# Performance work log

Measured on AMD Instinct MI355X. Metric: run time of the kernel, lower is better.

## Reference

```python
import jax, jax.numpy as jnp
import numpy as np

NUM_PHRASE = 8
HDIM = 256
NUM_HEADS = 8
NUM_LAYERS = 3
MIN_DIST = 2


def sine_pos(mask, num_feats, temperature=10000.0):
    # PositionEmbeddingSine (1D, DETR-style, normalize=False)
    B, L = mask.shape
    x_embed = jnp.cumsum(mask.astype(jnp.float32), axis=1)            # [B,L]
    dim_t = jnp.arange(num_feats, dtype=jnp.float32)
    dim_t = temperature ** (2.0 * jnp.floor(dim_t / 2.0) / num_feats)
    pos = x_embed[:, :, None] / dim_t                                  # [B,L,C]
    pos = jnp.stack([jnp.sin(pos[:, :, 0::2]), jnp.cos(pos[:, :, 1::2])], axis=3)
    return pos.reshape(B, L, num_feats)


def layer_norm(x, g, b, eps=1e-5):
    mu = jnp.mean(x, axis=-1, keepdims=True)
    var = jnp.mean((x - mu) ** 2, axis=-1, keepdims=True)
    return (x - mu) / jnp.sqrt(var + eps) * g + b


def mha(q, k, v, key_mask, in_w, in_b, out_w, out_b, nheads):
    # torch nn.MultiheadAttention (batch_first, eval/no-dropout), averaged attn weights
    B, Lq, C = q.shape
    Dh = C // nheads
    qp = (q @ in_w[:, :C] + in_b[:C]).reshape(B, Lq, nheads, Dh)
    kp = (k @ in_w[:, C:2 * C] + in_b[C:2 * C]).reshape(B, -1, nheads, Dh)
    vp = (v @ in_w[:, 2 * C:] + in_b[2 * C:]).reshape(B, -1, nheads, Dh)
    scores = jnp.einsum('bqhd,bkhd->bhqk', qp, kp) / jnp.sqrt(jnp.float32(Dh))
    scores = jnp.where(key_mask[:, None, None, :], scores, -jnp.inf)
    attn = jax.nn.softmax(scores, axis=-1)
    out = jnp.einsum('bhqk,bkhd->bqhd', attn, vp).reshape(B, Lq, C)
    return out @ out_w + out_b, jnp.mean(attn, axis=1)


def cross_attention(x, y, mask, qw, qb, kvw, kvb, inw, inb, ow, ob, g0, b0, lw, lb, g1, b1):
    C = x.shape[-1]
    q = x @ qw + qb
    kv = y @ kvw + kvb
    k, v = kv[..., :C], kv[..., C:]
    q_att, attn = mha(q, k, v, mask, inw, inb, ow, ob, NUM_HEADS)
    x = layer_norm(x + q_att, g0, b0)
    update = jax.nn.relu(x @ lw + lb)
    x = layer_norm(x + update, g1, b1)
    return x, attn


def _select_one(entropy_b, mask_b):
    # greedy highest-entropy selection with min-distance suppression (1D NMS)
    P, MD = NUM_PHRASE, MIN_DIST
    score = jnp.where(mask_b, entropy_b, -jnp.inf)
    order = jnp.argsort(-score).astype(jnp.int32)   # valid indices first, descending entropy

    def step(carry, idx):
        sel, cnt = carry
        dists = jnp.where(sel >= 0, jnp.abs(idx - sel), 1000000)
        ok = mask_b[idx] & (cnt < P) & (jnp.min(dists) >= MD)
        new_sel = jnp.where(ok, sel.at[jnp.minimum(cnt, P - 1)].set(idx), sel)
        return (new_sel, cnt + ok.astype(jnp.int32)), None

    init = (jnp.full((P,), -1, jnp.int32), jnp.int32(0))
    (sel, cnt), _ = jax.lax.scan(step, init, order)
    last = sel[jnp.maximum(cnt - 1, 0)]
    return jnp.where(jnp.arange(P) < cnt, sel, last)   # pad by repeating last


def phrase_generate(txt_emb, txt_mask, video_feats, video_mask,
                    word_proj_w, word_proj_b, video_proj_w, video_proj_b,
                    q_w, q_b, kv_w, kv_b, in_w, in_b, out_w, out_b,
                    ln0_g, ln0_b, lin_w, lin_b, ln1_g, ln1_b, eos_slot):
    B, L, C = txt_emb.shape
    word_emb = txt_emb[:, 1:]
    word_mask = txt_mask[:, 1:]
    word_pe = word_emb + sine_pos(word_mask, C)

    # word importance via video cross-attention entropy
    wp = word_pe @ word_proj_w + word_proj_b                      # [B,Lw,C]
    vp = video_feats @ video_proj_w + video_proj_b                # [B,T,C]
    sim = jnp.einsum('blc,btc->blt', wp, vp)                      # [B,Lw,T]
    sim = jnp.where(video_mask[:, None, :], sim, -jnp.inf)
    attn_weights = jax.nn.softmax(sim, axis=2)
    entropy = -jnp.sum(attn_weights * jnp.log(attn_weights + 1e-6), axis=2)  # [B,Lw]

    sel = jax.vmap(_select_one)(entropy, word_mask)               # [B,P] int32
    phrase_slot = jnp.take_along_axis(word_pe, sel[:, :, None], axis=1)      # [B,P,C]

    slot_sim = None
    for i in range(NUM_LAYERS):
        phrase_slot, slot_sim = cross_attention(
            phrase_slot, word_pe, word_mask,
            q_w[i], q_b[i], kv_w[i], kv_b[i], in_w[i], in_b[i], out_w[i], out_b[i],
            ln0_g[i], ln0_b[i], lin_w[i], lin_b[i], ln1_g[i], ln1_b[i])

    eos = jnp.broadcast_to(eos_slot, (B, 1, C))
    return phrase_slot, attn_weights, slot_sim, eos


def setup_inputs() -> dict:
    key = jax.random.key(0)
    ks = jax.random.split(key, 16)
    B, L, T, C, NL = 128, 257, 1024, HDIM, NUM_LAYERS
    s = 0.02
    inp = {
        'txt_emb': jax.random.normal(ks[0], (B, L, C), jnp.float32),
        'txt_mask': jnp.ones((B, L), jnp.bool_),
        'video_feats': jax.random.normal(ks[1], (B, T, C), jnp.float32),
        'video_mask': jnp.ones((B, T), jnp.bool_),
        'word_proj_w': jax.random.normal(ks[2], (C, C)) * s,
        'word_proj_b': jnp.zeros((C,)),
        'video_proj_w': jax.random.normal(ks[3], (C, C)) * s,
        'video_proj_b': jnp.zeros((C,)),
        'q_w': jax.random.normal(ks[4], (NL, C, C)) * s,
        'q_b': jnp.zeros((NL, C)),
        'kv_w': jax.random.normal(ks[5], (NL, C, 2 * C)) * s,
        'kv_b': jnp.zeros((NL, 2 * C)),
        'in_w': jax.random.normal(ks[6], (NL, C, 3 * C)) * s,
        'in_b': jnp.zeros((NL, 3 * C)),
        'out_w': jax.random.normal(ks[7], (NL, C, C)) * s,
        'out_b': jnp.zeros((NL, C)),
        'ln0_g': jnp.ones((NL, C)),
        'ln0_b': jnp.zeros((NL, C)),
        'lin_w': jax.random.normal(ks[8], (NL, C, C)) * s,
        'lin_b': jnp.zeros((NL, C)),
        'ln1_g': jnp.ones((NL, C)),
        'ln1_b': jnp.zeros((NL, C)),
        'eos_slot': jax.random.normal(ks[9], (1, 1, C)),
    }
    return inp


def reference(txt_emb, txt_mask, video_feats, video_mask,
              word_proj_w, word_proj_b, video_proj_w, video_proj_b,
              q_w, q_b, kv_w, kv_b, in_w, in_b, out_w, out_b,
              ln0_g, ln0_b, lin_w, lin_b, ln1_g, ln1_b, eos_slot):
    return phrase_generate(txt_emb, txt_mask, video_feats, video_mask,
                           word_proj_w, word_proj_b, video_proj_w, video_proj_b,
                           q_w, q_b, kv_w, kv_b, in_w, in_b, out_w, out_b,
                           ln0_g, ln0_b, lin_w, lin_b, ln1_g, ln1_b, eos_slot)
```

## Files before the change

kernel.cpp:

```cpp
#include <hip/hip_runtime.h>
#include <math.h>

#define BB 128
#define LFULL 257
#define LW 256
#define TT 1024
#define CC 256
#define NH 8
#define DHD 32
#define PP 8
#define NLAY 3

typedef __bf16 bf16x8 __attribute__((ext_vector_type(8)));
typedef __bf16 bf16x4 __attribute__((ext_vector_type(4)));
typedef float  f32x4  __attribute__((ext_vector_type(4)));

__device__ __forceinline__ float blockReduceSum(float v, volatile float* lds) {
#pragma unroll
    for (int m = 32; m >= 1; m >>= 1) v += __shfl_xor(v, m);
    __syncthreads();
    if ((threadIdx.x & 63) == 0) lds[threadIdx.x >> 6] = v;
    __syncthreads();
    return lds[0] + lds[1] + lds[2] + lds[3];
}
__device__ __forceinline__ float blockReduceMax(float v, volatile float* lds) {
#pragma unroll
    for (int m = 32; m >= 1; m >>= 1) v = fmaxf(v, __shfl_xor(v, m));
    __syncthreads();
    if ((threadIdx.x & 63) == 0) lds[threadIdx.x >> 6] = v;
    __syncthreads();
    return fmaxf(fmaxf(lds[0], lds[1]), fmaxf(lds[2], lds[3]));
}


__device__ __forceinline__ int ldsoff(int row, int col) {
    return ((row >> 6) << 11)
         + ((((row >> 4) & 3) << 2) + (col >> 3)) * 128
         + ((row & 15) << 3) + (col & 7);
}

template<int SPLIT, int B_F32, int OUT_SPLIT>
__global__ __launch_bounds__(512, 4) void gemm_mfma(
    const __bf16* __restrict__ Ahi, const __bf16* __restrict__ Alo, int lda, long long sA,
    const void* __restrict__ Bhp, const void* __restrict__ Blp, int ldb, long long sB,
    const float* __restrict__ bias,
    float* __restrict__ Cf, __bf16* __restrict__ Chi, __bf16* __restrict__ Clo,
    int ldc, long long sC, int M, int N, int K)
{
    __shared__ __bf16 sAh[2][4096];
    __shared__ __bf16 sAl[SPLIT ? 2 : 1][SPLIT ? 4096 : 1];
    __shared__ __bf16 sBh[2][4096];
    __shared__ __bf16 sBl[SPLIT ? 2 : 1][SPLIT ? 4096 : 1];

    const int tid = threadIdx.x;
    const int n0 = blockIdx.x * 128;
    const int m0 = blockIdx.y * 128;
    const long long bz = blockIdx.z;
    const __bf16* Ah = Ahi + bz * sA;
    const __bf16* Al = SPLIT ? (Alo + bz * sA) : nullptr;

    const int wv = tid >> 6, lane = tid & 63;
    const int wm = (wv & 1) << 6;
    const int wn = (wv >> 1) << 5;
    const int lr = lane & 15, quad = lane >> 4;

    const int sr = tid >> 2;
    const int sc = (tid & 3) << 3;
    const int soff = ldsoff(sr, sc);
    const long long aoff = (long long)(m0 + sr) * lda + sc;
    const long long boff = (long long)(n0 + sr) * ldb + sc;

    const int abase = ((wm >> 6) << 11) + (lane << 3);
    const int bbase = ((wn >> 6) << 11) + (((wn >> 4) & 3) << 9) + (lane << 3);

    bf16x8 rAh0, rAl0, rBh0, rBl0; float4 rBa0, rBb0;
    bf16x8 rAh1, rAl1, rBh1, rBl1; float4 rBa1, rBb1;

#define LOADR(S, k0) do {                                                         \
    rAh##S = *(const bf16x8*)&Ah[aoff + (k0)];                                    \
    if constexpr (SPLIT) rAl##S = *(const bf16x8*)&Al[aoff + (k0)];               \
    if constexpr (B_F32) {                                                        \
        const float* Bf_ = (const float*)Bhp + bz * sB;                           \
        rBa##S = *(const float4*)&Bf_[boff + (k0)];                               \
        rBb##S = *(const float4*)&Bf_[boff + (k0) + 4];                           \
    } else {                                                                      \
        const __bf16* Bh_ = (const __bf16*)Bhp + bz * sB;                         \
        rBh##S = *(const bf16x8*)&Bh_[boff + (k0)];                               \
        if constexpr (SPLIT) {                                                    \
            const __bf16* Bl_ = (const __bf16*)Blp + bz * sB;                     \
            rBl##S = *(const bf16x8*)&Bl_[boff + (k0)];                           \
        }                                                                         \
    } } while (0)

#define WRITEL(S, buf) do {                                                       \
    *(bf16x8*)&sAh[buf][soff] = rAh##S;                                           \
    if constexpr (SPLIT) *(bf16x8*)&sAl[buf][soff] = rAl##S;                      \
    if constexpr (B_F32) {                                                        \
        bf16x8 h8_, l8_;                                                          \
        h8_[0] = (__bf16)rBa##S.x; l8_[0] = (__bf16)(rBa##S.x - (float)h8_[0]);   \
        h8_[1] = (__bf16)rBa##S.y; l8_[1] = (__bf16)(rBa##S.y - (float)h8_[1]);   \
        h8_[2] = (__bf16)rBa##S.z; l8_[2] = (__bf16)(rBa##S.z - (float)h8_[2]);   \
        h8_[3] = (__bf16)rBa##S.w; l8_[3] = (__bf16)(rBa##S.w - (float)h8_[3]);   \
        h8_[4] = (__bf16)rBb##S.x; l8_[4] = (__bf16)(rBb##S.x - (float)h8_[4]);   \
        h8_[5] = (__bf16)rBb##S.y; l8_[5] = (__bf16)(rBb##S.y - (float)h8_[5]);   \
        h8_[6] = (__bf16)rBb##S.z; l8_[6] = (__bf16)(rBb##S.z - (float)h8_[6]);   \
        h8_[7] = (__bf16)rBb##S.w; l8_[7] = (__bf16)(rBb##S.w - (float)h8_[7]);   \
        *(bf16x8*)&sBh[buf][soff] = h8_;                                          \
        *(bf16x8*)&sBl[buf][soff] = l8_;                                          \
    } else {                                                                      \
        *(bf16x8*)&sBh[buf][soff] = rBh##S;                                       \
        if constexpr (SPLIT) *(bf16x8*)&sBl[buf][soff] = rBl##S;                  \
    } } while (0)

    f32x4 acc[4][2];
#pragma unroll
    for (int i = 0; i < 4; ++i)
#pragma unroll
        for (int j = 0; j < 2; ++j) acc[i][j] = (f32x4)(0.f);

    auto DOMFMA = [&](int buf) {
        bf16x8 fbh[2], fbl[2];
#pragma unroll
        for (int j = 0; j < 2; ++j) {
            fbh[j] = *(const bf16x8*)&sBh[buf][bbase + j * 512];
            if constexpr (SPLIT)
                fbl[j] = *(const bf16x8*)&sBl[buf][bbase + j * 512];
        }
#pragma unroll
        for (int i = 0; i < 4; ++i) {
            bf16x8 fah = *(const bf16x8*)&sAh[buf][abase + i * 512];
            if constexpr (SPLIT) {
                bf16x8 fal = *(const bf16x8*)&sAl[buf][abase + i * 512];
#pragma unroll
                for (int j = 0; j < 2; ++j) {
                    acc[i][j] = __builtin_amdgcn_mfma_f32_16x16x32_bf16(fal, fbh[j], acc[i][j], 0, 0, 0);
                    acc[i][j] = __builtin_amdgcn_mfma_f32_16x16x32_bf16(fah, fbl[j], acc[i][j], 0, 0, 0);
                    acc[i][j] = __builtin_amdgcn_mfma_f32_16x16x32_bf16(fah, fbh[j], acc[i][j], 0, 0, 0);
                }
            } else {
#pragma unroll
                for (int j = 0; j < 2; ++j)
                    acc[i][j] = __builtin_amdgcn_mfma_f32_16x16x32_bf16(fah, fbh[j], acc[i][j], 0, 0, 0);
            }
        }
    };

    const int nt = K >> 5;
    LOADR(0, 0);
    if (nt > 1) LOADR(1, 32);
    WRITEL(0, 0);
    if (nt > 2) LOADR(0, 64);
    __syncthreads();

    for (int t = 0; t < nt; t += 2) {
        DOMFMA(0);
        if (t + 1 < nt) {
            WRITEL(1, 1);
            if (t + 3 < nt) LOADR(1, (t + 3) << 5);
            __syncthreads();
            DOMFMA(1);
            if (t + 2 < nt) {
                WRITEL(0, 0);
                if (t + 4 < nt) LOADR(0, (t + 4) << 5);
                __syncthreads();
            }
        }
    }
#undef LOADR
#undef WRITEL

#pragma unroll
    for (int i = 0; i < 4; ++i)
#pragma unroll
        for (int j = 0; j < 2; ++j) {
            int col = n0 + wn + j * 16 + lr;
            int row0 = m0 + wm + i * 16 + quad * 4;
            float bv = bias ? bias[col] : 0.f;
#pragma unroll
            for (int r = 0; r < 4; ++r) {
                float v = acc[i][j][r] + bv;
                long long off = (long long)(row0 + r) * ldc + col + bz * sC;
                if constexpr (OUT_SPLIT) {
                    __bf16 h = (__bf16)v;
                    Chi[off] = h;
                    Clo[off] = (__bf16)(v - (float)h);
                } else {
                    Cf[off] = v;
                }
            }
        }
}

#define GTS 64
#define GKT 16
#define GPAD 68

template<int TRANSB, int RELU, int TRANSC>
__global__ __launch_bounds__(256) void gemm_f32(
    const float* __restrict__ A, int lda, long long sA,
    const float* __restrict__ Bm, int ldb, long long sB,
    const float* __restrict__ bias,
    float* __restrict__ C, int ldc, long long sC,
    int M, int N, int K)
{
    __shared__ float As[GKT][GPAD];
    __shared__ float Bs[GKT][GPAD];
    const int tid = threadIdx.x;
    const int tx = tid & 15, ty = tid >> 4;
    const int n0 = blockIdx.x * GTS;
    const int m0 = blockIdx.y * GTS;
    const long long bz = blockIdx.z;
    const float* Ab = A + bz * sA;
    const float* Bb = Bm + bz * sB;
    float* Cb = C + bz * sC;

    const int lr = tid >> 2;
    const int lc = (tid & 3) << 2;
    const int br = tid >> 4;
    const int bc = (tid & 15) << 2;

    float acc[4][4] = {};

    for (int k0 = 0; k0 < K; k0 += GKT) {
        float4 a = *(const float4*)&Ab[(long long)(m0 + lr) * lda + k0 + lc];
        As[lc + 0][lr] = a.x; As[lc + 1][lr] = a.y;
        As[lc + 2][lr] = a.z; As[lc + 3][lr] = a.w;
        if (TRANSB) {
            float4 b = *(const float4*)&Bb[(long long)(n0 + lr) * ldb + k0 + lc];
            Bs[lc + 0][lr] = b.x; Bs[lc + 1][lr] = b.y;
            Bs[lc + 2][lr] = b.z; Bs[lc + 3][lr] = b.w;
        } else {
            float4 b = *(const float4*)&Bb[(long long)(k0 + br) * ldb + n0 + bc];
            *(float4*)&Bs[br][bc] = b;
        }
        __syncthreads();
#pragma unroll
        for (int k = 0; k < GKT; ++k) {
            float4 av = *(const float4*)&As[k][ty << 2];
            float4 bv = *(const float4*)&Bs[k][tx << 2];
            float ar[4] = {av.x, av.y, av.z, av.w};
            float brr[4] = {bv.x, bv.y, bv.z, bv.w};
#pragma unroll
            for (int i = 0; i < 4; ++i)
#pragma unroll
                for (int j = 0; j < 4; ++j)
                    acc[i][j] = fmaf(ar[i], brr[j], acc[i][j]);
        }
        __syncthreads();
    }

    float bbr[4] = {0.f, 0.f, 0.f, 0.f};
    if (bias) {
        float4 bb = *(const float4*)&bias[n0 + (tx << 2)];
        bbr[0] = bb.x; bbr[1] = bb.y; bbr[2] = bb.z; bbr[3] = bb.w;
    }
#pragma unroll
    for (int i = 0; i < 4; ++i) {
#pragma unroll
        for (int j = 0; j < 4; ++j) {
            float o = acc[i][j] + bbr[j];
            if (RELU) o = fmaxf(o, 0.f);
            if (TRANSC)
                Cb[(long long)(n0 + (tx << 2) + j) * ldc + m0 + (ty << 2) + i] = o;
            else
                Cb[(long long)(m0 + (ty << 2) + i) * ldc + n0 + (tx << 2) + j] = o;
        }
    }
}


__global__ __launch_bounds__(256) void cumsum_kernel(
    const int* __restrict__ tm, int* __restrict__ cums)
{
    int b = blockIdx.x, c = threadIdx.x;
    int lane = c & 63;
    int v = (tm[(long long)b * LFULL + 1 + c] != 0) ? 1 : 0;
#pragma unroll
    for (int off = 1; off < 64; off <<= 1) {
        int t = __shfl_up(v, off);
        if (lane >= off) v += t;
    }
    __shared__ int wsum[4];
    if (lane == 63) wsum[c >> 6] = v;
    __syncthreads();
    int w = c >> 6, add = 0;
    for (int i = 0; i < w; ++i) add += wsum[i];
    cums[b * LW + c] = v + add;
}

__global__ __launch_bounds__(256) void pe_table_kernel(float* __restrict__ petab)
{
    int n = blockIdx.x;
    int c = threadIdx.x;
    int i2 = c & ~1;
    float freq = powf(10000.0f, (float)i2 / (float)CC);
    float arg = (float)n / freq;
    petab[n * CC + c] = (c & 1) ? cosf(arg) : sinf(arg);
}

__global__ __launch_bounds__(256) void word_pe2_kernel(
    const float* __restrict__ te, const int* __restrict__ cums,
    const float* __restrict__ petab,
    __bf16* __restrict__ whi, __bf16* __restrict__ wlo)
{
    int g = blockIdx.x * 256 + threadIdx.x;
    int c0 = (g & 63) << 2;
    int l  = (g >> 6) & 255;
    int b  = g >> 14;
    int cnt = cums[b * LW + l];
    float4 s = *(const float4*)&te[((long long)(b * LFULL + 1 + l)) * CC + c0];
    float4 p = *(const float4*)&petab[cnt * CC + c0];
    float v0 = s.x + p.x, v1 = s.y + p.y, v2 = s.z + p.z, v3 = s.w + p.w;
    bf16x4 h, lo;
    h[0] = (__bf16)v0; lo[0] = (__bf16)(v0 - (float)h[0]);
    h[1] = (__bf16)v1; lo[1] = (__bf16)(v1 - (float)h[1]);
    h[2] = (__bf16)v2; lo[2] = (__bf16)(v2 - (float)h[2]);
    h[3] = (__bf16)v3; lo[3] = (__bf16)(v3 - (float)h[3]);
    long long o = ((long long)(b * LW + l)) * CC + c0;
    *(bf16x4*)&whi[o] = h;
    *(bf16x4*)&wlo[o] = lo;
}

__global__ __launch_bounds__(256) void split_transpose_kernel(
    const float* __restrict__ W, __bf16* __restrict__ hi, __bf16* __restrict__ lo)
{
    int n = blockIdx.x, k = threadIdx.x;
    float v = W[(long long)k * CC + n];
    __bf16 h = (__bf16)v;
    hi[(long long)n * CC + k] = h;
    lo[(long long)n * CC + k] = (__bf16)(v - (float)h);
}
__global__ __launch_bounds__(256) void split_plain_kernel(
    const float* __restrict__ W, __bf16* __restrict__ hi, __bf16* __restrict__ lo)
{
    int g = blockIdx.x * 256 + threadIdx.x;
    float v = W[g];
    __bf16 h = (__bf16)v;
    hi[g] = h;
    lo[g] = (__bf16)(v - (float)h);
}
__global__ __launch_bounds__(256) void cvt_bf16_kernel(
    const float* __restrict__ src, __bf16* __restrict__ dst)
{
    int g = blockIdx.x * 256 + threadIdx.x;
    dst[g] = (__bf16)src[g];
}

__global__ __launch_bounds__(256) void softmax_entropy_kernel(
    float* __restrict__ attn, const int* __restrict__ vmask,
    float* __restrict__ ent)
{
    __shared__ float lds[4];
    long long row = blockIdx.x;
    int b = blockIdx.x >> 8;
    float* p = attn + row * TT;
    const int* m = vmask + (long long)b * TT;
    int t4 = threadIdx.x * 4;
    float4 v = *(const float4*)&p[t4];
    int4 mm4 = *(const int4*)&m[t4];
    float x[4];
    x[0] = mm4.x ? v.x : -INFINITY;
    x[1] = mm4.y ? v.y : -INFINITY;
    x[2] = mm4.z ? v.z : -INFINITY;
    x[3] = mm4.w ? v.w : -INFINITY;
    float mx = fmaxf(fmaxf(x[0], x[1]), fmaxf(x[2], x[3]));
    mx = blockReduceMax(mx, lds);
    float e[4];
    float ps = 0.f;
#pragma unroll
    for (int j = 0; j < 4; ++j) { e[j] = expf(x[j] - mx); ps += e[j]; }
    float sum = blockReduceSum(ps, lds);
    float q[4];
    float ce = 0.f;
#pragma unroll
    for (int j = 0; j < 4; ++j) {
        q[j] = e[j] / sum;
        ce += q[j] * logf(q[j] + 1e-6f);
    }
    ce = blockReduceSum(ce, lds);
    *(float4*)&p[t4] = make_float4(q[0], q[1], q[2], q[3]);
    if (threadIdx.x == 0) ent[row] = -ce;
}

__global__ __launch_bounds__(256) void select_kernel(
    const float* __restrict__ ent, const int* __restrict__ tm,
    int* __restrict__ sel)
{
    int b = blockIdx.x;
    int l = threadIdx.x;
    __shared__ float sc[LW];
    __shared__ int ord[LW];
    __shared__ unsigned char mk[LW];
    mk[l] = (tm[(long long)b * LFULL + 1 + l] != 0);
    sc[l] = mk[l] ? ent[(long long)b * LW + l] : -INFINITY;
    __syncthreads();
    float mys = sc[l];
    int r = 0;
    for (int j = 0; j < LW; ++j) {
        float s = sc[j];
        r += (s > mys) || (s == mys && j < l);
    }
    ord[r] = l;
    __syncthreads();
    if (l == 0) {
        int chosen[PP];
        int cnt = 0;
        for (int t = 0; t < LW; ++t) {
            int idx = ord[t];
            if (!mk[idx]) continue;
            if (cnt >= PP) break;
            bool ok = true;
            for (int s2 = 0; s2 < cnt; ++s2) {
                int d = idx - chosen[s2];
                if (d < 0) d = -d;
                if (d < 2) ok = false;
            }
            if (ok) chosen[cnt++] = idx;
        }
        int last = (cnt > 0) ? chosen[cnt - 1] : -1;
        for (int p = 0; p < PP; ++p)
            sel[b * PP + p] = (p < cnt) ? chosen[p] : last;
    }
}

__global__ __launch_bounds__(256) void gather_kernel(
    const __bf16* __restrict__ whi, const __bf16* __restrict__ wlo,
    const int* __restrict__ sel, float* __restrict__ x0)
{
    int g = blockIdx.x * 256 + threadIdx.x;
    int b = g >> 11;
    int p = (g >> 8) & 7;
    int c = g & 255;
    int idx = sel[b * PP + p];
    if (idx < 0) idx = 0;
    long long off = ((long long)b * LW + idx) * CC + c;
    x0[g] = (float)whi[off] + (float)wlo[off];
}

__global__ __launch_bounds__(256) void eff_bias_kernel(
    const float* __restrict__ q_b, const float* __restrict__ kv_b,
    const float* __restrict__ in_w, const float* __restrict__ in_b,
    float* __restrict__ BQE_all, float* __restrict__ bkv3)
{
    int i = blockIdx.x / 3;
    int role = blockIdx.x % 3;
    int n = threadIdx.x;
    const float* inw = in_w + (long long)i * 196608;
    const float* inb = in_b + (long long)i * 768;
    const float* srcb;
    int co;
    float* dst;
    if (role == 0)      { srcb = q_b + i * 256;        co = 0;   dst = BQE_all + i * 256; }
    else if (role == 1) { srcb = kv_b + i * 512;       co = 256; dst = bkv3 + i * 512; }
    else                { srcb = kv_b + i * 512 + 256; co = 512; dst = bkv3 + i * 512 + 256; }
    float s = inb[co + n];
#pragma unroll 8
    for (int k = 0; k < CC; ++k)
        s = fmaf(srcb[k], inw[(long long)k * 768 + co + n], s);
    dst[n] = s;
}

__global__ __launch_bounds__(256) void attn_scores_kernel(
    const float* __restrict__ qp, const float* __restrict__ KV,
    const int* __restrict__ tm, float* __restrict__ attn)
{
    int b = blockIdx.x, h = blockIdx.y;
    int tid = threadIdx.x;
    __shared__ float qs[PP][DHD];
    __shared__ float sc[PP][LW];
    __shared__ float mxs[PP], sms[PP];
    {
        int q = tid >> 5, d = tid & 31;
        qs[q][d] = qp[((long long)(b * PP + q)) * CC + h * DHD + d];
    }
    __syncthreads();
    const float* kr = KV + ((long long)(b * LW + tid)) * 512 + h * DHD;
    float kreg[DHD];
#pragma unroll
    for (int j = 0; j < 8; ++j) {
        float4 f = *(const float4*)&kr[j * 4];
        kreg[j * 4 + 0] = f.x; kreg[j * 4 + 1] = f.y;
        kreg[j * 4 + 2] = f.z; kreg[j * 4 + 3] = f.w;
    }
    bool mk = tm[(long long)b * LFULL + 1 + tid] != 0;
#pragma unroll
    for (int q = 0; q < PP; ++q) {
        float s = 0.f;
#pragma unroll
        for (int d = 0; d < DHD; ++d) s = fmaf(qs[q][d], kreg[d], s);
        sc[q][tid] = mk ? s * 0.17677669529663687f : -INFINITY;
    }
    __syncthreads();
    {
        int q = tid >> 5, j = tid & 31;
        float m = -INFINITY;
        for (int kk = j; kk < LW; kk += 32) m = fmaxf(m, sc[q][kk]);
#pragma unroll
        for (int mm = 16; mm >= 1; mm >>= 1) m = fmaxf(m, __shfl_xor(m, mm, 32));
        float s = 0.f;
        for (int kk = j; kk < LW; kk += 32) s += expf(sc[q][kk] - m);
#pragma unroll
        for (int mm = 16; mm >= 1; mm >>= 1) s += __shfl_xor(s, mm, 32);
        if (j == 0) { mxs[q] = m; sms[q] = s; }
    }
    __syncthreads();
#pragma unroll
    for (int q = 0; q < PP; ++q) {
        float pv = expf(sc[q][tid] - mxs[q]) / sms[q];
        attn[(((long long)(b * NH + h)) * PP + q) * LW + tid] = pv;
    }
}

__global__ __launch_bounds__(256) void attn_out_kernel(
    const float* __restrict__ attn, const float* __restrict__ KV,
    float* __restrict__ aout)
{
    int b = blockIdx.x, q = blockIdx.y;
    int c = threadIdx.x, h = c >> 5;
    __shared__ float att[NH][LW];
#pragma unroll
    for (int hh = 0; hh < NH; ++hh)
        att[hh][c] = attn[(((long long)(b * NH + hh)) * PP + q) * LW + c];
    __syncthreads();
    const float* vpb = KV + ((long long)b * LW) * 512 + 256 + c;
    float acc = 0.f;
#pragma unroll 8
    for (int k = 0; k < LW; ++k)
        acc = fmaf(att[h][k], vpb[(long long)k * 512], acc);
    aout[((long long)(b * PP + q)) * CC + c] = acc;
}

__global__ __launch_bounds__(256) void slot_sim_kernel(
    const float* __restrict__ attn, float* __restrict__ outs)
{
    int b = blockIdx.x, q = blockIdx.y, k = threadIdx.x;
    float s = 0.f;
#pragma unroll
    for (int h = 0; h < NH; ++h)
        s += attn[(((long long)(b * NH + h)) * PP + q) * LW + k];
    outs[((long long)(b * PP + q)) * LW + k] = s * 0.125f;
}

__global__ __launch_bounds__(256) void ln_residual_kernel(
    const float* __restrict__ xin, const float* __restrict__ add,
    const float* __restrict__ g, const float* __restrict__ bta,
    float* __restrict__ out)
{
    __shared__ float lds[4];
    int r = blockIdx.x, c = threadIdx.x;
    long long idx = (long long)r * CC + c;
    float v = xin[idx] + add[idx];
    float s = blockReduceSum(v, lds);
    float mu = s * (1.0f / (float)CC);
    float d = v - mu;
    float var = blockReduceSum(d * d, lds) * (1.0f / (float)CC);
    out[idx] = d / sqrtf(var + 1e-5f) * g[c] + bta[c];
}

__global__ __launch_bounds__(256) void eos_kernel(
    const float* __restrict__ eos, float* __restrict__ outp)
{
    outp[(long long)blockIdx.x * CC + threadIdx.x] = eos[threadIdx.x];
}

extern "C" void kernel_launch(void* const* d_in, const int* in_sizes, int n_in,
                              void* d_out, int out_size, void* d_ws, size_t ws_size,
                              hipStream_t stream) {
    const float* txt_emb     = (const float*)d_in[0];
    const int*   txt_mask    = (const int*)d_in[1];
    const float* video_feats = (const float*)d_in[2];
    const int*   video_mask  = (const int*)d_in[3];
    const float* word_proj_w = (const float*)d_in[4];
    const float* word_proj_b = (const float*)d_in[5];
    const float* video_proj_w = (const float*)d_in[6];
    const float* q_w   = (const float*)d_in[8];
    const float* q_b   = (const float*)d_in[9];
    const float* kv_w  = (const float*)d_in[10];
    const float* kv_b  = (const float*)d_in[11];
    const float* in_w  = (const float*)d_in[12];
    const float* in_b  = (const float*)d_in[13];
    const float* out_w = (const float*)d_in[14];
    const float* out_b = (const float*)d_in[15];
    const float* ln0_g = (const float*)d_in[16];
    const float* ln0_b = (const float*)d_in[17];
    const float* lin_w = (const float*)d_in[18];
    const float* lin_b = (const float*)d_in[19];
    const float* ln1_g = (const float*)d_in[20];
    const float* ln1_b = (const float*)d_in[21];
    const float* eos_slot = (const float*)d_in[22];

    float* ws = (float*)d_ws;
    __bf16* wpe_hi = (__bf16*)(ws + 0LL);
    __bf16* wpe_lo = (__bf16*)(ws + 4194304LL);
    __bf16* wp_hi  = (__bf16*)(ws + 8388608LL);
    __bf16* wp_lo  = (__bf16*)(ws + 12582912LL);
    __bf16* U_hi   = (__bf16*)(ws + 16777216LL);
    __bf16* U_lo   = (__bf16*)(ws + 20971520LL);
    float*  KV     = ws + 8388608LL;
    float* ent     = ws + 25165824LL;
    int*   sel     = (int*)(ws + 25198592LL);
    float* x0      = ws + 25199616LL;
    float* x1      = ws + 25461760LL;
    float* xmid    = ws + 25723904LL;
    float* qp      = ws + 25986048LL;
    float* attnw   = ws + 26248192LL;
    float* aout    = ws + 28345344LL;
    float* qatt    = ws + 28607488LL;
    float* upd     = ws + 28869632LL;
    float* WQE_all = ws + 29131776LL;
    float* BQE_all = ws + 29328384LL;
    float* WT3f    = ws + 29329152LL;
    __bf16* WT3    = (__bf16*)(ws + 29722368LL);
    float* bkv3    = ws + 29918976LL;
    __bf16* WPT_hi = (__bf16*)(ws + 29920512LL);
    __bf16* WPT_lo = (__bf16*)(ws + 29953280LL);
    __bf16* VPS_hi = (__bf16*)(ws + 29986048LL);
    __bf16* VPS_lo = (__bf16*)(ws + 30018816LL);

    int*   cums  = (int*)(ws + 8388608LL);
    float* petab = ws + 8421376LL;

    float* outp     = (float*)d_out;
    float* out_ps   = outp;
    float* out_attn = outp + 262144LL;
    float* out_slot = outp + 33816576LL;
    float* out_eos  = outp + 34078720LL;

    cumsum_kernel<<<dim3(BB), dim3(256), 0, stream>>>(txt_mask, cums);
    pe_table_kernel<<<dim3(257), dim3(256), 0, stream>>>(petab);
    word_pe2_kernel<<<dim3(8192), dim3(256), 0, stream>>>(txt_emb, cums, petab, wpe_hi, wpe_lo);
    split_transpose_kernel<<<dim3(256), dim3(256), 0, stream>>>(word_proj_w, WPT_hi, WPT_lo);
    split_plain_kernel<<<dim3(256), dim3(256), 0, stream>>>(video_proj_w, VPS_hi, VPS_lo);
    gemm_mfma<1,0,1><<<dim3(2,256,1), dim3(512), 0, stream>>>(
        wpe_hi, wpe_lo, 256, 0, WPT_hi, WPT_lo, 256, 0, word_proj_b,
        nullptr, wp_hi, wp_lo, 256, 0, 32768, 256, 256);
    gemm_mfma<1,0,1><<<dim3(2,256,1), dim3(512), 0, stream>>>(
        wp_hi, wp_lo, 256, 0, VPS_hi, VPS_lo, 256, 0, nullptr,
        nullptr, U_hi, U_lo, 256, 0, 32768, 256, 256);
    gemm_mfma<1,1,0><<<dim3(8,2,BB), dim3(512), 0, stream>>>(
        U_hi, U_lo, 256, 65536LL, video_feats, nullptr, 256, 262144LL, nullptr,
        out_attn, nullptr, nullptr, 1024, 262144LL, 256, 1024, 256);
    softmax_entropy_kernel<<<dim3(32768), dim3(256), 0, stream>>>(out_attn, video_mask, ent);
    select_kernel<<<dim3(BB), dim3(256), 0, stream>>>(ent, txt_mask, sel);
    gather_kernel<<<dim3(1024), dim3(256), 0, stream>>>(wpe_hi, wpe_lo, sel, x0);

    gemm_f32<0,0,0><<<dim3(4,4,3), dim3(256), 0, stream>>>(
        q_w,256,65536LL, in_w,768,196608LL, nullptr, WQE_all,256,65536LL, 256,256,256);
    gemm_f32<0,0,1><<<dim3(4,4,3), dim3(256), 0, stream>>>(
        kv_w,512,131072LL, in_w+256,768,196608LL, nullptr, WT3f,256,131072LL, 256,256,256);
    gemm_f32<0,0,1><<<dim3(4,4,3), dim3(256), 0, stream>>>(
        kv_w+256,512,131072LL, in_w+512,768,196608LL, nullptr, WT3f+65536,256,131072LL, 256,256,256);
    eff_bias_kernel<<<dim3(9), dim3(256), 0, stream>>>(q_b, kv_b, in_w, in_b, BQE_all, bkv3);
    cvt_bf16_kernel<<<dim3(1536), dim3(256), 0, stream>>>(WT3f, (__bf16*)WT3);

    float* X = x0;
    for (int i = 0; i < NLAY; ++i) {
        const float* ow  = out_w + (long long)i * 65536;
        const float* ob  = out_b + (long long)i * 256;
        const float* g0  = ln0_g + (long long)i * 256;
        const float* b0  = ln0_b + (long long)i * 256;
        const float* lw  = lin_w + (long long)i * 65536;
        const float* lb  = lin_b + (long long)i * 256;
        const float* g1  = ln1_g + (long long)i * 256;
        const float* b1  = ln1_b + (long long)i * 256;

        gemm_mfma<0,0,0><<<dim3(4,256,1), dim3(512), 0, stream>>>(
            wpe_hi, nullptr, 256, 0, WT3 + (long long)i * 131072, nullptr, 256, 0,
            bkv3 + i * 512, KV, nullptr, nullptr, 512, 0, 32768, 512, 256);

        gemm_f32<0,0,0><<<dim3(4,16,1), dim3(256), 0, stream>>>(
            X,256,0, WQE_all + (long long)i*65536,256,0, BQE_all + i*256, qp,256,0, 1024,256,256);

        attn_scores_kernel<<<dim3(BB,NH), dim3(256), 0, stream>>>(qp, KV, txt_mask, attnw);
        attn_out_kernel<<<dim3(BB,PP), dim3(256), 0, stream>>>(attnw, KV, aout);
        if (i == NLAY - 1)
            slot_sim_kernel<<<dim3(BB,PP), dim3(256), 0, stream>>>(attnw, out_slot);

        gemm_f32<0,0,0><<<dim3(4,16,1), dim3(256), 0, stream>>>(
            aout,256,0, ow,256,0, ob, qatt,256,0, 1024,256,256);
        ln_residual_kernel<<<dim3(1024), dim3(256), 0, stream>>>(X, qatt, g0, b0, xmid);
        gemm_f32<0,1,0><<<dim3(4,16,1), dim3(256), 0, stream>>>(
            xmid,256,0, lw,256,0, lb, upd,256,0, 1024,256,256);
        float* Xout = (i == NLAY - 1) ? out_ps : ((X == x0) ? x1 : x0);
        ln_residual_kernel<<<dim3(1024), dim3(256), 0, stream>>>(xmid, upd, g1, b1, Xout);
        X = Xout;
    }
    eos_kernel<<<dim3(BB), dim3(256), 0, stream>>>(eos_slot, out_eos);
}
```

Baseline: 889.9 us.

## Fuse similarity GEMM with masked softmax and entropy into one kernel

Replaces the batched similarity GEMM plus the separate softmax/entropy pass with a single kernel. Each 1024-thread block computes a 32x1024 score tile in registers with split-bf16 MFMAs, then does the masked softmax and entropy reductions through shuffles and LDS before writing the probabilities once. This removes a full write and read-back of the 128x256x1024 fp32 attention tensor and one kernel launch. In exchange, each block holds a full row of 1024 columns, so there is one block per 32 rows, every block re-reads its batch's video features, and the large block size may limit occupancy.

```diff
diff --git a/kernel.cpp b/kernel.cpp
--- a/kernel.cpp
+++ b/kernel.cpp
@@ -191,6 +191,204 @@
         }
 }
 
+__global__ __launch_bounds__(1024, 4) void sim_fused_kernel(
+    const __bf16* __restrict__ Uhi, const __bf16* __restrict__ Ulo,
+    const float* __restrict__ video, const int* __restrict__ vmask,
+    float* __restrict__ attn, float* __restrict__ ent)
+{
+    __shared__ __bf16 sAh[8192];
+    __shared__ __bf16 sAl[8192];
+    __shared__ float red[16][32];
+
+    const int tid = threadIdx.x;
+    const int m0 = blockIdx.x * 32;
+    const long long z = blockIdx.y;
+    const int wv = tid >> 6, lane = tid & 63;
+    const int lr = lane & 15, quad = lane >> 4;
+    const int wn = wv << 6;
+
+    const __bf16* Ah = Uhi + z * 65536;
+    const __bf16* Al = Ulo + z * 65536;
+    const float*  Bf = video + z * 262144;
+
+    {
+        int srow = (((tid >> 6) & 1) << 4) + (tid & 15);
+        int sk0  = ((tid >> 7) << 5) + (((tid >> 4) & 3) << 3);
+        long long goff = (long long)(m0 + srow) * CC + sk0;
+        *(bf16x8*)&sAh[tid * 8] = *(const bf16x8*)&Ah[goff];
+        *(bf16x8*)&sAl[tid * 8] = *(const bf16x8*)&Al[goff];
+    }
+
+    bool mk[4];
+#pragma unroll
+    for (int j = 0; j < 4; ++j)
+        mk[j] = vmask[z * TT + wn + j * 16 + lr] != 0;
+
+    f32x4 acc[2][4];
+#pragma unroll
+    for (int mf = 0; mf < 2; ++mf)
+#pragma unroll
+        for (int j = 0; j < 4; ++j) acc[mf][j] = (f32x4)(0.f);
+
+    __syncthreads();
+
+    const long long bb = (long long)(wn + lr) * CC + quad * 8;
+#pragma unroll
+    for (int ks = 0; ks < 8; ++ks) {
+        float4 b0[4], b1[4];
+#pragma unroll
+        for (int j = 0; j < 4; ++j) {
+            const float* p = Bf + bb + j * 4096 + ks * 32;
+            b0[j] = *(const float4*)p;
+            b1[j] = *(const float4*)(p + 4);
+        }
+        bf16x8 fah[2], fal[2];
+#pragma unroll
+        for (int mf = 0; mf < 2; ++mf) {
+            fah[mf] = *(const bf16x8*)&sAh[ks * 1024 + mf * 512 + lane * 8];
+            fal[mf] = *(const bf16x8*)&sAl[ks * 1024 + mf * 512 + lane * 8];
+        }
+#pragma unroll
+        for (int j = 0; j < 4; ++j) {
+            bf16x8 bh, bl;
+            bh[0] = (__bf16)b0[j].x; bl[0] = (__bf16)(b0[j].x - (float)bh[0]);
+            bh[1] = (__bf16)b0[j].y; bl[1] = (__bf16)(b0[j].y - (float)bh[1]);
+            bh[2] = (__bf16)b0[j].z; bl[2] = (__bf16)(b0[j].z - (float)bh[2]);
+            bh[3] = (__bf16)b0[j].w; bl[3] = (__bf16)(b0[j].w - (float)bh[3]);
+            bh[4] = (__bf16)b1[j].x; bl[4] = (__bf16)(b1[j].x - (float)bh[4]);
+            bh[5] = (__bf16)b1[j].y; bl[5] = (__bf16)(b1[j].y - (float)bh[5]);
+            bh[6] = (__bf16)b1[j].z; bl[6] = (__bf16)(b1[j].z - (float)bh[6]);
+            bh[7] = (__bf16)b1[j].w; bl[7] = (__bf16)(b1[j].w - (float)bh[7]);
+#pragma unroll
+            for (int mf = 0; mf < 2; ++mf) {
+                acc[mf][j] = __builtin_amdgcn_mfma_f32_16x16x32_bf16(fal[mf], bh, acc[mf][j], 0, 0, 0);
+                acc[mf][j] = __builtin_amdgcn_mfma_f32_16x16x32_bf16(fah[mf], bl, acc[mf][j], 0, 0, 0);
+                acc[mf][j] = __builtin_amdgcn_mfma_f32_16x16x32_bf16(fah[mf], bh, acc[mf][j], 0, 0, 0);
+            }
+        }
+    }
+
+    float pmax[2][4];
+#pragma unroll
+    for (int mf = 0; mf < 2; ++mf)
+#pragma unroll
+        for (int rr = 0; rr < 4; ++rr) {
+            float m = -INFINITY;
+#pragma unroll
+            for (int j = 0; j < 4; ++j)
+                if (mk[j]) m = fmaxf(m, acc[mf][j][rr]);
+            pmax[mf][rr] = m;
+        }
+#pragma unroll
+    for (int d = 1; d < 16; d <<= 1)
+#pragma unroll
+        for (int mf = 0; mf < 2; ++mf)
+#pragma unroll
+            for (int rr = 0; rr < 4; ++rr)
+                pmax[mf][rr] = fmaxf(pmax[mf][rr], __shfl_xor(pmax[mf][rr], d));
+    if (lr == 0)
+#pragma unroll
+        for (int mf = 0; mf < 2; ++mf)
+#pragma unroll
+            for (int rr = 0; rr < 4; ++rr)
+                red[wv][mf * 16 + quad * 4 + rr] = pmax[mf][rr];
+    __syncthreads();
+    float rmax[2][4];
+#pragma unroll
+    for (int mf = 0; mf < 2; ++mf)
+#pragma unroll
+        for (int rr = 0; rr < 4; ++rr) {
+            float m = -INFINITY;
+            for (int w = 0; w < 16; ++w) m = fmaxf(m, red[w][mf * 16 + quad * 4 + rr]);
+            rmax[mf][rr] = m;
+        }
+    __syncthreads();
+
+    float psum[2][4];
+#pragma unroll
+    for (int mf = 0; mf < 2; ++mf)
+#pragma unroll
+        for (int rr = 0; rr < 4; ++rr) psum[mf][rr] = 0.f;
+#pragma unroll
+    for (int mf = 0; mf < 2; ++mf)
+#pragma unroll
+        for (int j = 0; j < 4; ++j)
+#pragma unroll
+            for (int rr = 0; rr < 4; ++rr) {
+                float xv = mk[j] ? acc[mf][j][rr] : -INFINITY;
+                float ev = expf(xv - rmax[mf][rr]);
+                acc[mf][j][rr] = ev;
+                psum[mf][rr] += ev;
+            }
+#pragma unroll
+    for (int d = 1; d < 16; d <<= 1)
+#pragma unroll
+        for (int mf = 0; mf < 2; ++mf)
+#pragma unroll
+            for (int rr = 0; rr < 4; ++rr)
+                psum[mf][rr] += __shfl_xor(psum[mf][rr], d);
+    if (lr == 0)
+#pragma unroll
+        for (int mf = 0; mf < 2; ++mf)
+#pragma unroll
+            for (int rr = 0; rr < 4; ++rr)
+                red[wv][mf * 16 + quad * 4 + rr] = psum[mf][rr];
+    __syncthreads();
+    float rsum[2][4];
+#pragma unroll
+    for (int mf = 0; mf < 2; ++mf)
+#pragma unroll
+        for (int rr = 0; rr < 4; ++rr) {
+            float s = 0.f;
+            for (int w = 0; w < 16; ++w) s += red[w][mf * 16 + quad * 4 + rr];
+            rsum[mf][rr] = s;
+        }
+    __syncthreads();
+
+    float pce[2][4];
+#pragma unroll
+    for (int mf = 0; mf < 2; ++mf)
+#pragma unroll
+        for (int rr = 0; rr < 4; ++rr) pce[mf][rr] = 0.f;
+#pragma unroll
+    for (int mf = 0; mf < 2; ++mf)
+#pragma unroll
+        for (int rr = 0; rr < 4; ++rr) {
+            long long rowg = z * (long long)LW + m0 + mf * 16 + quad * 4 + rr;
+#pragma unroll
+            for (int j = 0; j < 4; ++j) {
+                float q = acc[mf][j][rr] / rsum[mf][rr];
+                attn[rowg * TT + wn + j * 16 + lr] = q;
+                pce[mf][rr] += q * logf(q + 1e-6f);
+            }
+        }
+#pragma unroll
+    for (int d = 1; d < 16; d <<= 1)
+#pragma unroll
+        for (int mf = 0; mf < 2; ++mf)
+#pragma unroll
+            for (int rr = 0; rr < 4; ++rr)
+                pce[mf][rr] += __shfl_xor(pce[mf][rr], d);
+    if (lr == 0)
+#pragma unroll
+        for (int mf = 0; mf < 2; ++mf)
+#pragma unroll
+            for (int rr = 0; rr < 4; ++rr)
+                red[wv][mf * 16 + quad * 4 + rr] = pce[mf][rr];
+    __syncthreads();
+    if (wv == 0 && lr == 0) {
+#pragma unroll
+        for (int mf = 0; mf < 2; ++mf)
+#pragma unroll
+            for (int rr = 0; rr < 4; ++rr) {
+                int row = mf * 16 + quad * 4 + rr;
+                float s = 0.f;
+                for (int w = 0; w < 16; ++w) s += red[w][row];
+                ent[z * (long long)LW + m0 + row] = -s;
+            }
+    }
+}
+
 #define GTS 64
 #define GKT 16
 #define GPAD 68
@@ -267,7 +465,6 @@
         }
     }
 }
-
 
 __global__ __launch_bounds__(256) void cumsum_kernel(
     const int* __restrict__ tm, int* __restrict__ cums)
@@ -344,42 +541,6 @@
 {
     int g = blockIdx.x * 256 + threadIdx.x;
     dst[g] = (__bf16)src[g];
-}
-
-__global__ __launch_bounds__(256) void softmax_entropy_kernel(
-    float* __restrict__ attn, const int* __restrict__ vmask,
-    float* __restrict__ ent)
-{
-    __shared__ float lds[4];
-    long long row = blockIdx.x;
-    int b = blockIdx.x >> 8;
-    float* p = attn + row * TT;
-    const int* m = vmask + (long long)b * TT;
-    int t4 = threadIdx.x * 4;
-    float4 v = *(const float4*)&p[t4];
-    int4 mm4 = *(const int4*)&m[t4];
-    float x[4];
-    x[0] = mm4.x ? v.x : -INFINITY;
-    x[1] = mm4.y ? v.y : -INFINITY;
-    x[2] = mm4.z ? v.z : -INFINITY;
-    x[3] = mm4.w ? v.w : -INFINITY;
-    float mx = fmaxf(fmaxf(x[0], x[1]), fmaxf(x[2], x[3]));
-    mx = blockReduceMax(mx, lds);
-    float e[4];
-    float ps = 0.f;
-#pragma unroll
-    for (int j = 0; j < 4; ++j) { e[j] = expf(x[j] - mx); ps += e[j]; }
-    float sum = blockReduceSum(ps, lds);
-    float q[4];
-    float ce = 0.f;
-#pragma unroll
-    for (int j = 0; j < 4; ++j) {
-        q[j] = e[j] / sum;
-        ce += q[j] * logf(q[j] + 1e-6f);
-    }
-    ce = blockReduceSum(ce, lds);
-    *(float4*)&p[t4] = make_float4(q[0], q[1], q[2], q[3]);
-    if (threadIdx.x == 0) ent[row] = -ce;
 }
 
 __global__ __launch_bounds__(256) void select_kernel(
@@ -637,10 +798,8 @@
     gemm_mfma<1,0,1><<<dim3(2,256,1), dim3(512), 0, stream>>>(
         wp_hi, wp_lo, 256, 0, VPS_hi, VPS_lo, 256, 0, nullptr,
         nullptr, U_hi, U_lo, 256, 0, 32768, 256, 256);
-    gemm_mfma<1,1,0><<<dim3(8,2,BB), dim3(512), 0, stream>>>(
-        U_hi, U_lo, 256, 65536LL, video_feats, nullptr, 256, 262144LL, nullptr,
-        out_attn, nullptr, nullptr, 1024, 262144LL, 256, 1024, 256);
-    softmax_entropy_kernel<<<dim3(32768), dim3(256), 0, stream>>>(out_attn, video_mask, ent);
+    sim_fused_kernel<<<dim3(8, BB), dim3(1024), 0, stream>>>(
+        U_hi, U_lo, video_feats, video_mask, out_attn, ent);
     select_kernel<<<dim3(BB), dim3(256), 0, stream>>>(ent, txt_mask, sel);
     gather_kernel<<<dim3(1024), dim3(256), 0, stream>>>(wpe_hi, wpe_lo, sel, x0);
 
```

Result: slower. 1.013 ms (+13.9%).
